# Kernel optimization log

Measured on AMD Instinct MI355X. Metric: run time of the kernel, lower is better.

## Reference

```python
import jax, jax.numpy as jnp
import numpy as np

B, S, D, H = 2, 2048, 1024, 16
HD = D // H  # head_dim = 64
ROPE_BASE = 10000.0
NEG_MIN = jnp.finfo(jnp.float32).min


def _rope_cos_sin(seq_len, head_dim):
    inv_freq = 1.0 / (ROPE_BASE ** (jnp.arange(0, head_dim, 2, dtype=jnp.float32) / head_dim))
    t = jnp.arange(seq_len, dtype=jnp.float32)
    freqs = jnp.einsum('i,j->ij', t, inv_freq)           # [S, HD/2]
    emb = jnp.concatenate([freqs, freqs], axis=-1)        # [S, HD]
    return jnp.cos(emb), jnp.sin(emb)


def _rotate_half(x):
    x1, x2 = jnp.split(x, 2, axis=-1)
    return jnp.concatenate([-x2, x1], axis=-1)


def setup_inputs() -> dict:
    key = jax.random.key(0)
    ks = jax.random.split(key, 5)
    sc = 0.02
    hidden_states = jax.random.normal(ks[0], (B, S, D), dtype=jnp.float32)
    wq = jax.random.normal(ks[1], (D, D), dtype=jnp.float32) * sc
    wk = jax.random.normal(ks[2], (D, D), dtype=jnp.float32) * sc
    wv = jax.random.normal(ks[3], (D, D), dtype=jnp.float32) * sc
    wo = jax.random.normal(ks[4], (D, D), dtype=jnp.float32) * sc
    # additive causal mask [B,1,S,S]: 0 on/below diagonal, large negative above
    causal = jnp.tril(jnp.ones((S, S), dtype=jnp.bool_))
    attention_mask = jnp.where(causal, 0.0, NEG_MIN)[None, None, :, :].astype(jnp.float32)
    attention_mask = jnp.broadcast_to(attention_mask, (B, 1, S, S))
    position_ids = jnp.broadcast_to(jnp.arange(S, dtype=jnp.int32)[None, :], (B, S))
    return {"hidden_states": hidden_states, "attention_mask": attention_mask,
            "wq": wq, "wk": wk, "wv": wv, "wo": wo, "position_ids": position_ids}


def reference(hidden_states, attention_mask, wq, wk, wv, wo, position_ids):
    bsz, q_len, _ = hidden_states.shape

    def shape_heads(x):
        return x.reshape(bsz, q_len, H, HD).transpose(0, 2, 1, 3)  # [B,H,S,HD]

    q = shape_heads(hidden_states @ wq)
    k = shape_heads(hidden_states @ wk)
    v = shape_heads(hidden_states @ wv)

    cos, sin = _rope_cos_sin(q_len, HD)                   # [S, HD]
    cos = cos[position_ids][:, None, :, :]                # [B,1,S,HD]
    sin = sin[position_ids][:, None, :, :]
    q = q * cos + _rotate_half(q) * sin
    k = k * cos + _rotate_half(k) * sin

    scores = jnp.einsum('bhqd,bhkd->bhqk', q, k) / jnp.sqrt(jnp.float32(HD))
    scores = jnp.maximum(scores + attention_mask, NEG_MIN)
    attn = jax.nn.softmax(scores, axis=-1)
    out = jnp.einsum('bhqk,bhkd->bhqd', attn, v)          # [B,H,S,HD]
    out = out.transpose(0, 2, 1, 3).reshape(bsz, q_len, D)
    return out @ wo
```

## Files before the change

### kernel.cpp

```cpp
#include <hip/hip_runtime.h>

#define B_ 2
#define S_ 2048
#define D_ 1024
#define H_ 16
#define HD_ 64

typedef unsigned short u16;
typedef __attribute__((ext_vector_type(8))) short short8;
typedef __attribute__((ext_vector_type(4))) float f32x4;

__device__ __forceinline__ u16 f2bf(float f) {
  union { float f; unsigned u; } v; v.f = f;
  unsigned r = v.u + 0x7fffu + ((v.u >> 16) & 1u);
  return (u16)(r >> 16);
}
__device__ __forceinline__ float bf2f(u16 b) {
  union { unsigned u; float f; } v; v.u = ((unsigned)b) << 16;
  return v.f;
}
__device__ __forceinline__ unsigned pkbf(float a, float b) {
  return (unsigned)f2bf(a) | ((unsigned)f2bf(b) << 16);
}
__device__ __forceinline__ void gload_lds16(const u16* g, u16* l) {
  __builtin_amdgcn_global_load_lds((const __attribute__((address_space(1))) void*)g,
                                   (__attribute__((address_space(3))) void*)l, 16, 0, 0);
}

__global__ __launch_bounds__(256) void prep_kernel(const float* __restrict__ hs,
                                                   const float* __restrict__ W0,
                                                   const float* __restrict__ W1,
                                                   const float* __restrict__ W2,
                                                   const float* __restrict__ W3,
                                                   u16* __restrict__ Xb,
                                                   u16* __restrict__ WT) {
  __shared__ float T[64][65];
  if (blockIdx.z == 4) {
    const int base = (blockIdx.y * 16 + blockIdx.x) * 4096 + threadIdx.x;
#pragma unroll 4
    for (int i = 0; i < 16; ++i) {
      const int idx = base + i * 256;
      const float4 v = ((const float4*)hs)[idx];
      ushort4 o;
      o.x = f2bf(v.x); o.y = f2bf(v.y); o.z = f2bf(v.z); o.w = f2bf(v.w);
      ((ushort4*)Xb)[idx] = o;
    }
    return;
  }
  const float* Wz[4] = {W0, W1, W2, W3};
  const float* W = Wz[blockIdx.z];
  u16* dst = WT + (size_t)blockIdx.z * (1024 * 1024);
  const int nb = blockIdx.x * 64, kb = blockIdx.y * 64;
  const int t = threadIdx.x;
  const int r = t >> 2, c4 = (t & 3) * 16;
#pragma unroll
  for (int i = 0; i < 4; ++i) {
    float4 v = *(const float4*)&W[(kb + r) * D_ + nb + c4 + i * 4];
    T[r][c4 + i * 4 + 0] = v.x;
    T[r][c4 + i * 4 + 1] = v.y;
    T[r][c4 + i * 4 + 2] = v.z;
    T[r][c4 + i * 4 + 3] = v.w;
  }
  __syncthreads();
#pragma unroll
  for (int i = 0; i < 4; ++i) {
    ushort4 o;
    o.x = f2bf(T[c4 + i * 4 + 0][r]);
    o.y = f2bf(T[c4 + i * 4 + 1][r]);
    o.z = f2bf(T[c4 + i * 4 + 2][r]);
    o.w = f2bf(T[c4 + i * 4 + 3][r]);
    *(ushort4*)&dst[(nb + r) * D_ + kb + c4 + i * 4] = o;
  }
}

template <int BN, int MODE, int DB>
__global__ __launch_bounds__(256) void gemm_kernel(const u16* __restrict__ A,
                                                   const u16* __restrict__ BT,
                                                   float* __restrict__ out0,
                                                   u16* __restrict__ oQ,
                                                   u16* __restrict__ oK,
                                                   u16* __restrict__ oV,
                                                   const int* __restrict__ posarr) {
  constexpr int K = D_;
  constexpr int NT = BN / 32;
  constexpr int BI = BN / 32;
  constexpr int ABANK = 128 * 64;
  constexpr int BBANK = BN * 64;
  constexpr int STAGE = (DB + 1) * (ABANK + BBANK);
  constexpr int EPIU = (MODE == 1) ? 128 * 136 : 0;
  constexpr int SMU = STAGE > EPIU ? STAGE : EPIU;
  __shared__ u16 smem[SMU];
  u16* AsP = smem;
  u16* BsP = smem + (DB + 1) * ABANK;

  const int t = threadIdx.x, lane = t & 63, w = t >> 6;
  const int l15 = lane & 15, quad = lane >> 4;
  const int n0 = blockIdx.x * BN, m0 = blockIdx.y * 128;
  const int wm = (w >> 1) * 64, wn = (w & 1) * (BN / 2);

  f32x4 acc[4][NT];
#pragma unroll
  for (int mt = 0; mt < 4; ++mt)
#pragma unroll
    for (int nt = 0; nt < NT; ++nt) acc[mt][nt] = (f32x4){0.f, 0.f, 0.f, 0.f};

  const u16* ag[4]; int aoff[4];
  const u16* bg[BI]; int boff[BI];
#pragma unroll
  for (int j = 0; j < 4; ++j) {
    int slot = w * 256 + j * 64 + lane;
    int row = slot >> 3, q = (slot & 7) ^ (row & 7);
    ag[j] = A + (size_t)(m0 + row) * K + q * 8;
    aoff[j] = (w * 256 + j * 64) * 8;
  }
#pragma unroll
  for (int j = 0; j < BI; ++j) {
    int slot = w * (BI * 64) + j * 64 + lane;
    int row = slot >> 3, q = (slot & 7) ^ (row & 7);
    bg[j] = BT + (size_t)(n0 + row) * K + q * 8;
    boff[j] = (w * (BI * 64) + j * 64) * 8;
  }

  auto stage = [&](int k0, int buf) {
#pragma unroll
    for (int j = 0; j < 4; ++j) gload_lds16(ag[j] + k0, AsP + buf * ABANK + aoff[j]);
#pragma unroll
    for (int j = 0; j < BI; ++j) gload_lds16(bg[j] + k0, BsP + buf * BBANK + boff[j]);
  };
  auto compute = [&](int buf) {
    const u16* Ab = AsP + buf * ABANK;
    const u16* Bb = BsP + buf * BBANK;
#pragma unroll
    for (int kc = 0; kc < 2; ++kc) {
      short8 af[4], bf[NT];
#pragma unroll
      for (int mt = 0; mt < 4; ++mt) {
        int row = wm + mt * 16 + l15;
        af[mt] = *(const short8*)&Ab[row * 64 + (((kc * 4 + quad) ^ (row & 7)) * 8)];
      }
#pragma unroll
      for (int nt = 0; nt < NT; ++nt) {
        int col = wn + nt * 16 + l15;
        bf[nt] = *(const short8*)&Bb[col * 64 + (((kc * 4 + quad) ^ (col & 7)) * 8)];
      }
#pragma unroll
      for (int mt = 0; mt < 4; ++mt)
#pragma unroll
        for (int nt = 0; nt < NT; ++nt)
          acc[mt][nt] = __builtin_amdgcn_mfma_f32_16x16x32_bf16(af[mt], bf[nt], acc[mt][nt], 0, 0, 0);
    }
  };

  if constexpr (DB == 0) {
    for (int k0 = 0; k0 < K; k0 += 64) {
      __syncthreads();
      stage(k0, 0);
      __syncthreads();
      compute(0);
    }
  } else {
    stage(0, 0);
#pragma unroll 1
    for (int it = 0; it < K / 64; ++it) {
      __syncthreads();
      if (it + 1 < K / 64) stage((it + 1) * 64, (it + 1) & 1);
      compute(it & 1);
    }
  }

  if (MODE == 0) {
#pragma unroll
    for (int mt = 0; mt < 4; ++mt) {
      const int row0 = m0 + wm + mt * 16 + quad * 4;
#pragma unroll
      for (int nt = 0; nt < NT; ++nt) {
        const int col = n0 + wn + nt * 16 + l15;
#pragma unroll
        for (int r = 0; r < 4; ++r) out0[(size_t)(row0 + r) * 1024 + col] = acc[mt][nt][r];
      }
    }
  } else {
    const int widx = n0 >> 10;
    if (widx == 2) {
      __syncthreads();
      u16* Epi = smem;
#pragma unroll
      for (int nt = 0; nt < NT; ++nt) {
        const int col = wn + nt * 16 + l15;
#pragma unroll
        for (int mt = 0; mt < 4; ++mt) {
          const int row0 = wm + mt * 16 + quad * 4;
          uint2 pk;
          pk.x = pkbf(acc[mt][nt][0], acc[mt][nt][1]);
          pk.y = pkbf(acc[mt][nt][2], acc[mt][nt][3]);
          *(uint2*)&Epi[col * 136 + row0] = pk;
        }
      }
      __syncthreads();
      const int col = t >> 1, half = t & 1;
      const int cc = (n0 + col) & 1023;
      const int h = cc >> 6, d = cc & 63;
      const int bb = m0 >> 11;
      const int s0 = (m0 & (S_ - 1)) + half * 64;
      u16* gp = oV + ((((size_t)(bb * H_ + h) * HD_ + d)) << 11) + s0;
#pragma unroll
      for (int i = 0; i < 8; ++i)
        ((uint4*)gp)[i] = *(const uint4*)&Epi[col * 136 + half * 64 + i * 8];
    } else {
      u16* dst = (widx == 0) ? oQ : oK;
      const float scale = (widx == 0) ? 0.125f : 1.0f;
      float invf[2];
      invf[0] = exp2f(-0.41524101186f * (float)l15);
      invf[1] = exp2f(-0.41524101186f * (float)(16 + l15));
      const int h = ((n0 + wn) & 1023) >> 6;
#pragma unroll
      for (int mt = 0; mt < 4; ++mt) {
        const int row0 = m0 + wm + mt * 16 + quad * 4;
#pragma unroll
        for (int r = 0; r < 4; ++r) {
          const int rw = row0 + r;
          const int b = rw >> 11, s = rw & (S_ - 1);
          const float pos = (float)posarr[b * S_ + s];
          const size_t base = (((size_t)(b * H_ + h) * S_ + s) << 6);
#pragma unroll
          for (int nt2 = 0; nt2 < 2; ++nt2) {
            float sn, c;
            __sincosf(pos * invf[nt2], &sn, &c);
            const float x1 = acc[mt][nt2][r], x2 = acc[mt][nt2 + 2][r];
            const int d = nt2 * 16 + l15;
            dst[base + d] = f2bf((x1 * c - x2 * sn) * scale);
            dst[base + d + 32] = f2bf((x2 * c + x1 * sn) * scale);
          }
        }
      }
    }
  }
}

__global__ __launch_bounds__(256, 4) void attn_kernel(const u16* __restrict__ Q,
                                                      const u16* __restrict__ Kx,
                                                      const u16* __restrict__ Vt,
                                                      u16* __restrict__ AO) {
  __shared__ u16 Ks[2][512 * 8];
  __shared__ u16 Vs[2][512 * 8];
  __shared__ u16 Pw[4][128 * 8];
  const int t = threadIdx.x;
  const int lane = t & 63, w = t >> 6;
  const int l15 = lane & 15, quad = lane >> 4;
  const int idx = blockIdx.x;
  const int bh = (idx & 7) | ((idx >> 8) << 3);
  const int qt = 31 - ((idx >> 3) & 31);
  const u16* qp = Q + bh * (S_ * HD_);
  const u16* kp = Kx + bh * (S_ * HD_);
  const u16* vp = Vt + bh * (HD_ * S_);
  const int wq16 = w * 16;
  const int q_lo = qt * 64 + wq16;

  int srow[2], sq[2];
#pragma unroll
  for (int jj = 0; jj < 2; ++jj) {
    int slot = w * 128 + jj * 64 + lane;
    srow[jj] = slot >> 3;
    sq[jj] = (slot & 7) ^ (srow[jj] & 7);
  }
  auto stage = [&](int kt, int buf) {
#pragma unroll
    for (int jj = 0; jj < 2; ++jj)
      gload_lds16(kp + (size_t)(kt * 64 + srow[jj]) * 64 + sq[jj] * 8,
                  &Ks[buf][(w * 128 + jj * 64) * 8]);
#pragma unroll
    for (int jj = 0; jj < 2; ++jj)
      gload_lds16(vp + (size_t)srow[jj] * S_ + kt * 64 + sq[jj] * 8,
                  &Vs[buf][(w * 128 + jj * 64) * 8]);
  };

  short8 qf[2];
#pragma unroll
  for (int kc = 0; kc < 2; ++kc)
    qf[kc] = *(const short8*)&qp[(q_lo + l15) * HD_ + kc * 32 + quad * 8];

  f32x4 o[4];
  float m_ = -INFINITY, l_ = 0.f;
#pragma unroll
  for (int i = 0; i < 4; ++i) o[i] = (f32x4){0.f, 0.f, 0.f, 0.f};

  stage(0, 0);
  for (int kt = 0; kt <= qt; ++kt) {
    __syncthreads();
    if (kt < qt) stage(kt + 1, (kt + 1) & 1);
    const int buf = kt & 1;
    short8 kf[8], vf[8];
#pragma unroll
    for (int kc = 0; kc < 2; ++kc)
#pragma unroll
      for (int nt = 0; nt < 4; ++nt) {
        const int row = nt * 16 + l15;
        kf[kc * 4 + nt] =
            *(const short8*)&Ks[buf][(row * 8 + ((kc * 4 + quad) ^ (row & 7))) * 8];
      }
#pragma unroll
    for (int dt = 0; dt < 4; ++dt)
#pragma unroll
      for (int kc = 0; kc < 2; ++kc) {
        const int row = dt * 16 + l15;
        vf[dt * 2 + kc] =
            *(const short8*)&Vs[buf][(row * 8 + ((kc * 4 + quad) ^ (row & 7))) * 8];
      }
    f32x4 sa[4];
#pragma unroll
    for (int i = 0; i < 4; ++i) sa[i] = (f32x4){0.f, 0.f, 0.f, 0.f};
#pragma unroll
    for (int kc = 0; kc < 2; ++kc)
#pragma unroll
      for (int nt = 0; nt < 4; ++nt)
        sa[nt] = __builtin_amdgcn_mfma_f32_16x16x32_bf16(kf[kc * 4 + nt], qf[kc], sa[nt], 0, 0, 0);
    if (kt == qt) {
#pragma unroll
      for (int nt = 0; nt < 4; ++nt)
#pragma unroll
        for (int r = 0; r < 4; ++r)
          if (nt * 16 + quad * 4 + r > wq16 + l15) sa[nt][r] = -INFINITY;
    }
    float mx = -INFINITY;
#pragma unroll
    for (int nt = 0; nt < 4; ++nt)
#pragma unroll
      for (int r = 0; r < 4; ++r) mx = fmaxf(mx, sa[nt][r]);
    mx = fmaxf(mx, __shfl_xor(mx, 16));
    mx = fmaxf(mx, __shfl_xor(mx, 32));
    const float mn = fmaxf(m_, mx);
    const float alpha = __expf(m_ - mn);
    m_ = mn;
    float p[16];
    float sum = 0.f;
#pragma unroll
    for (int nt = 0; nt < 4; ++nt)
#pragma unroll
      for (int r = 0; r < 4; ++r) {
        const float pe = __expf(sa[nt][r] - mn);
        p[nt * 4 + r] = pe;
        sum += pe;
      }
    sum += __shfl_xor(sum, 16);
    sum += __shfl_xor(sum, 32);
    l_ = l_ * alpha + sum;
#pragma unroll
    for (int dt = 0; dt < 4; ++dt)
#pragma unroll
      for (int r = 0; r < 4; ++r) o[dt][r] *= alpha;
#pragma unroll
    for (int nt = 0; nt < 4; ++nt) {
      const int q = nt * 2 + (quad >> 1);
      uint2 pk;
      pk.x = pkbf(p[nt * 4 + 0], p[nt * 4 + 1]);
      pk.y = pkbf(p[nt * 4 + 2], p[nt * 4 + 3]);
      *(uint2*)&Pw[w][(l15 * 8 + (q ^ (l15 & 7))) * 8 + (quad & 1) * 4] = pk;
    }
#pragma unroll
    for (int kc = 0; kc < 2; ++kc) {
      short8 pf = *(const short8*)&Pw[w][(l15 * 8 + (((kc * 4) + quad) ^ (l15 & 7))) * 8];
#pragma unroll
      for (int dt = 0; dt < 4; ++dt)
        o[dt] = __builtin_amdgcn_mfma_f32_16x16x32_bf16(vf[dt * 2 + kc], pf, o[dt], 0, 0, 0);
    }
  }

  const int b = bh >> 4, h = bh & 15;
  const float li = 1.0f / l_;
  const size_t base = ((size_t)(b * S_ + q_lo + l15)) * D_ + h * HD_;
#pragma unroll
  for (int dt = 0; dt < 4; ++dt)
#pragma unroll
    for (int rr = 0; rr < 2; ++rr)
      *(unsigned*)&AO[base + dt * 16 + quad * 4 + rr * 2] =
          pkbf(o[dt][rr * 2] * li, o[dt][rr * 2 + 1] * li);
}

extern "C" void kernel_launch(void* const* d_in, const int* in_sizes, int n_in,
                              void* d_out, int out_size, void* d_ws, size_t ws_size,
                              hipStream_t stream) {
  const float* hs = (const float*)d_in[0];
  const float* wq = (const float*)d_in[2];
  const float* wk = (const float*)d_in[3];
  const float* wv = (const float*)d_in[4];
  const float* wo = (const float*)d_in[5];
  const int* pos = (const int*)d_in[6];
  float* out = (float*)d_out;

  char* ws = (char*)d_ws;
  const size_t MB = (size_t)1 << 20;
  u16* Xb = (u16*)(ws);
  u16* WT = (u16*)(ws + 8 * MB);
  u16* Qh = (u16*)(ws + 16 * MB);
  u16* Kh = (u16*)(ws + 24 * MB);
  u16* Vt = (u16*)(ws + 32 * MB);
  u16* AO = (u16*)(ws + 40 * MB);

  prep_kernel<<<dim3(16, 16, 5), 256, 0, stream>>>(hs, wq, wk, wv, wo, Xb, WT);

  gemm_kernel<128, 1, 0><<<dim3(24, 32), 256, 0, stream>>>(Xb, WT, nullptr, Qh, Kh, Vt, pos);

  attn_kernel<<<1024, 256, 0, stream>>>(Qh, Kh, Vt, AO);

  gemm_kernel<128, 0, 1><<<dim3(8, 32), 256, 0, stream>>>(AO, WT + 3 * 1024 * 1024, out,
                                                          nullptr, nullptr, nullptr, nullptr);
}
```

Before: 231.6 us.

## Pair causal query tiles per block to share K loads and balance work

```diff
diff --git a/kernel.cpp b/kernel.cpp
--- a/kernel.cpp
+++ b/kernel.cpp
@@ -1,4 +1,5 @@
 #include <hip/hip_runtime.h>
+#include <hip/hip_bf16.h>
 
 #define B_ 2
 #define S_ 2048
@@ -10,17 +11,21 @@
 typedef __attribute__((ext_vector_type(8))) short short8;
 typedef __attribute__((ext_vector_type(4))) float f32x4;
 
+#if __has_builtin(__builtin_amdgcn_exp2f)
+#define EXP2F(x) __builtin_amdgcn_exp2f(x)
+#else
+#define EXP2F(x) exp2f(x)
+#endif
+
 __device__ __forceinline__ u16 f2bf(float f) {
   union { float f; unsigned u; } v; v.f = f;
   unsigned r = v.u + 0x7fffu + ((v.u >> 16) & 1u);
   return (u16)(r >> 16);
 }
-__device__ __forceinline__ float bf2f(u16 b) {
-  union { unsigned u; float f; } v; v.u = ((unsigned)b) << 16;
-  return v.f;
-}
 __device__ __forceinline__ unsigned pkbf(float a, float b) {
-  return (unsigned)f2bf(a) | ((unsigned)f2bf(b) << 16);
+  union { __hip_bfloat162 h; unsigned u; } v;
+  v.h = __float22bfloat162_rn(float2{a, b});
+  return v.u;
 }
 __device__ __forceinline__ void gload_lds16(const u16* g, u16* l) {
   __builtin_amdgcn_global_load_lds((const __attribute__((address_space(1))) void*)g,
@@ -208,7 +213,7 @@
         ((uint4*)gp)[i] = *(const uint4*)&Epi[col * 136 + half * 64 + i * 8];
     } else {
       u16* dst = (widx == 0) ? oQ : oK;
-      const float scale = (widx == 0) ? 0.125f : 1.0f;
+      const float scale = (widx == 0) ? 0.18033688011f : 1.0f;
       float invf[2];
       invf[0] = exp2f(-0.41524101186f * (float)l15);
       invf[1] = exp2f(-0.41524101186f * (float)(16 + l15));
@@ -237,24 +242,25 @@
   }
 }
 
-__global__ __launch_bounds__(256, 4) void attn_kernel(const u16* __restrict__ Q,
+__global__ __launch_bounds__(256, 2) void attn_kernel(const u16* __restrict__ Q,
                                                       const u16* __restrict__ Kx,
                                                       const u16* __restrict__ Vt,
                                                       u16* __restrict__ AO) {
-  __shared__ u16 Ks[2][512 * 8];
-  __shared__ u16 Vs[2][512 * 8];
+  __shared__ u16 Ks[2][2][512 * 8];
   __shared__ u16 Pw[4][128 * 8];
   const int t = threadIdx.x;
   const int lane = t & 63, w = t >> 6;
   const int l15 = lane & 15, quad = lane >> 4;
   const int idx = blockIdx.x;
-  const int bh = (idx & 7) | ((idx >> 8) << 3);
-  const int qt = 31 - ((idx >> 3) & 31);
+  const int pr = (idx >> 3) & 15;
+  const int bh = (idx & 7) | ((idx >> 7) << 3);
+  const int qtA = pr, qtB = 31 - pr;
   const u16* qp = Q + bh * (S_ * HD_);
   const u16* kp = Kx + bh * (S_ * HD_);
   const u16* vp = Vt + bh * (HD_ * S_);
   const int wq16 = w * 16;
-  const int q_lo = qt * 64 + wq16;
+  const int q_loA = qtA * 64 + wq16;
+  const int q_loB = qtB * 64 + wq16;
 
   int srow[2], sq[2];
 #pragma unroll
@@ -263,49 +269,53 @@
     srow[jj] = slot >> 3;
     sq[jj] = (slot & 7) ^ (srow[jj] & 7);
   }
-  auto stage = [&](int kt, int buf) {
+  auto stageK = [&](int kt, u16* dst) {
 #pragma unroll
     for (int jj = 0; jj < 2; ++jj)
       gload_lds16(kp + (size_t)(kt * 64 + srow[jj]) * 64 + sq[jj] * 8,
-                  &Ks[buf][(w * 128 + jj * 64) * 8]);
-#pragma unroll
-    for (int jj = 0; jj < 2; ++jj)
-      gload_lds16(vp + (size_t)srow[jj] * S_ + kt * 64 + sq[jj] * 8,
-                  &Vs[buf][(w * 128 + jj * 64) * 8]);
-  };
-
-  short8 qf[2];
-#pragma unroll
-  for (int kc = 0; kc < 2; ++kc)
-    qf[kc] = *(const short8*)&qp[(q_lo + l15) * HD_ + kc * 32 + quad * 8];
-
-  f32x4 o[4];
-  float m_ = -INFINITY, l_ = 0.f;
-#pragma unroll
-  for (int i = 0; i < 4; ++i) o[i] = (f32x4){0.f, 0.f, 0.f, 0.f};
-
-  stage(0, 0);
-  for (int kt = 0; kt <= qt; ++kt) {
-    __syncthreads();
-    if (kt < qt) stage(kt + 1, (kt + 1) & 1);
-    const int buf = kt & 1;
-    short8 kf[8], vf[8];
+                  dst + (w * 128 + jj * 64) * 8);
+  };
+  auto stageGroup = [&](int g, int buf) {
+    const int kt0 = g * 2;
+    stageK(kt0, &Ks[buf][0][0]);
+    if (kt0 + 1 <= qtB) stageK(kt0 + 1, &Ks[buf][1][0]);
+  };
+  auto loadKf = [&](int buf, int tt, short8* kf) {
 #pragma unroll
     for (int kc = 0; kc < 2; ++kc)
 #pragma unroll
       for (int nt = 0; nt < 4; ++nt) {
         const int row = nt * 16 + l15;
         kf[kc * 4 + nt] =
-            *(const short8*)&Ks[buf][(row * 8 + ((kc * 4 + quad) ^ (row & 7))) * 8];
-      }
+            *(const short8*)&Ks[buf][tt][(row * 8 + ((kc * 4 + quad) ^ (row & 7))) * 8];
+      }
+  };
+  auto loadV = [&](int kt, short8* vf) {
 #pragma unroll
     for (int dt = 0; dt < 4; ++dt)
 #pragma unroll
-      for (int kc = 0; kc < 2; ++kc) {
-        const int row = dt * 16 + l15;
+      for (int kc = 0; kc < 2; ++kc)
         vf[dt * 2 + kc] =
-            *(const short8*)&Vs[buf][(row * 8 + ((kc * 4 + quad) ^ (row & 7))) * 8];
-      }
+            *(const short8*)&vp[(dt * 16 + l15) * S_ + kt * 64 + kc * 32 + quad * 8];
+  };
+
+  short8 qfA[2], qfB[2];
+#pragma unroll
+  for (int kc = 0; kc < 2; ++kc) {
+    qfA[kc] = *(const short8*)&qp[(q_loA + l15) * HD_ + kc * 32 + quad * 8];
+    qfB[kc] = *(const short8*)&qp[(q_loB + l15) * HD_ + kc * 32 + quad * 8];
+  }
+
+  f32x4 oA[4], oB[4];
+  float mA = -INFINITY, lA = 0.f, mB = -INFINITY, lB = 0.f;
+#pragma unroll
+  for (int i = 0; i < 4; ++i) {
+    oA[i] = (f32x4){0.f, 0.f, 0.f, 0.f};
+    oB[i] = (f32x4){0.f, 0.f, 0.f, 0.f};
+  }
+
+  auto chainStep = [&](bool diag, const short8* qf, const short8* kf, const short8* vf,
+                       f32x4* o, float& m_, float& l_) {
     f32x4 sa[4];
 #pragma unroll
     for (int i = 0; i < 4; ++i) sa[i] = (f32x4){0.f, 0.f, 0.f, 0.f};
@@ -314,7 +324,7 @@
 #pragma unroll
       for (int nt = 0; nt < 4; ++nt)
         sa[nt] = __builtin_amdgcn_mfma_f32_16x16x32_bf16(kf[kc * 4 + nt], qf[kc], sa[nt], 0, 0, 0);
-    if (kt == qt) {
+    if (diag) {
 #pragma unroll
       for (int nt = 0; nt < 4; ++nt)
 #pragma unroll
@@ -329,7 +339,7 @@
     mx = fmaxf(mx, __shfl_xor(mx, 16));
     mx = fmaxf(mx, __shfl_xor(mx, 32));
     const float mn = fmaxf(m_, mx);
-    const float alpha = __expf(m_ - mn);
+    const float alpha = EXP2F(m_ - mn);
     m_ = mn;
     float p[16];
     float sum = 0.f;
@@ -337,7 +347,7 @@
     for (int nt = 0; nt < 4; ++nt)
 #pragma unroll
       for (int r = 0; r < 4; ++r) {
-        const float pe = __expf(sa[nt][r] - mn);
+        const float pe = EXP2F(sa[nt][r] - mn);
         p[nt * 4 + r] = pe;
         sum += pe;
       }
@@ -363,17 +373,43 @@
       for (int dt = 0; dt < 4; ++dt)
         o[dt] = __builtin_amdgcn_mfma_f32_16x16x32_bf16(vf[dt * 2 + kc], pf, o[dt], 0, 0, 0);
     }
+  };
+
+  const int ngroups = (qtB + 2) >> 1;
+  short8 vf0[8], vf1[8], kf[8];
+  stageGroup(0, 0);
+  loadV(0, vf0);
+#pragma unroll 1
+  for (int g = 0; g < ngroups; ++g) {
+    __syncthreads();
+    if (g + 1 < ngroups) stageGroup(g + 1, (g + 1) & 1);
+    const int buf = g & 1;
+    const int kt0 = 2 * g;
+    loadKf(buf, 0, kf);
+    if (kt0 + 1 <= qtB) loadV(kt0 + 1, vf1);
+    chainStep(kt0 == qtB, qfB, kf, vf0, oB, mB, lB);
+    if (kt0 <= qtA) chainStep(kt0 == qtA, qfA, kf, vf0, oA, mA, lA);
+    if (kt0 + 1 <= qtB) {
+      loadKf(buf, 1, kf);
+      if (kt0 + 2 <= qtB) loadV(kt0 + 2, vf0);
+      chainStep(kt0 + 1 == qtB, qfB, kf, vf1, oB, mB, lB);
+      if (kt0 + 1 <= qtA) chainStep(kt0 + 1 == qtA, qfA, kf, vf1, oA, mA, lA);
+    }
   }
 
   const int b = bh >> 4, h = bh & 15;
-  const float li = 1.0f / l_;
-  const size_t base = ((size_t)(b * S_ + q_lo + l15)) * D_ + h * HD_;
+  const float liA = 1.0f / lA, liB = 1.0f / lB;
+  const size_t baseA = ((size_t)(b * S_ + q_loA + l15)) * D_ + h * HD_;
+  const size_t baseB = ((size_t)(b * S_ + q_loB + l15)) * D_ + h * HD_;
 #pragma unroll
   for (int dt = 0; dt < 4; ++dt)
 #pragma unroll
-    for (int rr = 0; rr < 2; ++rr)
-      *(unsigned*)&AO[base + dt * 16 + quad * 4 + rr * 2] =
-          pkbf(o[dt][rr * 2] * li, o[dt][rr * 2 + 1] * li);
+    for (int rr = 0; rr < 2; ++rr) {
+      *(unsigned*)&AO[baseA + dt * 16 + quad * 4 + rr * 2] =
+          pkbf(oA[dt][rr * 2] * liA, oA[dt][rr * 2 + 1] * liA);
+      *(unsigned*)&AO[baseB + dt * 16 + quad * 4 + rr * 2] =
+          pkbf(oB[dt][rr * 2] * liB, oB[dt][rr * 2 + 1] * liB);
+    }
 }
 
 extern "C" void kernel_launch(void* const* d_in, const int* in_sizes, int n_in,
@@ -400,8 +436,8 @@
 
   gemm_kernel<128, 1, 0><<<dim3(24, 32), 256, 0, stream>>>(Xb, WT, nullptr, Qh, Kh, Vt, pos);
 
-  attn_kernel<<<1024, 256, 0, stream>>>(Qh, Kh, Vt, AO);
-
-  gemm_kernel<128, 0, 1><<<dim3(8, 32), 256, 0, stream>>>(AO, WT + 3 * 1024 * 1024, out,
+  attn_kernel<<<512, 256, 0, stream>>>(Qh, Kh, Vt, AO);
+
+  gemm_kernel<64, 0, 1><<<dim3(16, 32), 256, 0, stream>>>(AO, WT + 3 * 1024 * 1024, out,
                                                           nullptr, nullptr, nullptr, nullptr);
 }
```

Measured after the change: 230.4 us. About the same (-0.5%).
